# Optimization experiments

Hardware: AMD Instinct MI355X
Metric: run time of the kernel (lower is better)

Reference implementation:

```python
import jax, jax.numpy as jnp
import numpy as np

D = 128   # opt.geometric_latent_dim
H = 132   # FCBlock hidden width (hardcoded in source)
B = 65536
K = 8

def setup_inputs() -> dict:
    key = jax.random.key(0)
    ks = jax.random.split(key, 16)
    s = lambda k, shp, fan: jax.random.normal(k, shp, jnp.float32) / np.sqrt(fan)
    return {
        "signal": jax.random.normal(ks[0], (B, D), jnp.float32),
        "components": jax.random.normal(ks[1], (K, B, D), jnp.float32),
        # message_map / update_map: Linear(D, D)
        "Wm": s(ks[2], (D, D), D), "bm": jnp.zeros((D,), jnp.float32),
        "Wu": s(ks[3], (D, D), D), "bu": jnp.zeros((D,), jnp.float32),
        "W0": s(ks[4], (H, 2 * D), 2 * D), "b0": jnp.zeros((H,), jnp.float32),
        "W1": s(ks[5], (H, H), H),         "b1": jnp.zeros((H,), jnp.float32),
        "W2": s(ks[6], (H, H), H),         "b2": jnp.zeros((H,), jnp.float32),
        "W3": s(ks[7], (D, H), H),         "b3": jnp.zeros((D,), jnp.float32),
    }

def reference(signal, components, Wm, bm, Wu, bu, W0, b0, W1, b1, W2, b2, W3, b3):
    # message_map applied to each component, then summed over components
    msgs = jnp.einsum('kbd,ed->kbe', components, Wm) + bm  # [K,B,D]
    right = msgs.sum(axis=0)                               # [B,D]
    # update_map
    right = right @ Wu.T + bu                              # [B,D]
    # joint_update: FCBlock on concat([signal, right])
    x = jnp.concatenate([signal, right], axis=-1)          # [B,2D]
    x = jax.nn.relu(x @ W0.T + b0)
    x = jax.nn.relu(x @ W1.T + b1)
    x = jax.nn.relu(x @ W2.T + b2)
    return x @ W3.T + b3                                   # [B,D]
```

## Files before the change

### kernel.cpp

```cpp
#include <hip/hip_runtime.h>
#include <stdint.h>

#define DD  128
#define HH  132
#define BB  65536
#define KKC 8
#define HP  144
#define KP  160
#define SW  136
#define SH  168
#define W0S_BYTES 40960
#define WAB_BYTES 81920
#define WH_BYTES  49152
#define ACT_BYTES 43008

typedef short bf16x8 __attribute__((ext_vector_type(8)));
typedef short bf16x4 __attribute__((ext_vector_type(4)));
typedef float f32x4  __attribute__((ext_vector_type(4)));

__device__ __forceinline__ unsigned short f2b(float f){
  union{float f; unsigned u;} c; c.f = f;
  unsigned r = c.u + 0x7fffu + ((c.u >> 16) & 1u);
  return (unsigned short)(r >> 16);
}

__global__ void prepA(const float* __restrict__ Wm, const float* __restrict__ bm,
                      const float* __restrict__ Wu, const float* __restrict__ bu,
                      float* __restrict__ Wf, float* __restrict__ bfv){
  int idx = blockIdx.x * 256 + threadIdx.x;
  int i = idx >> 7, j = idx & 127;
  float acc = 0.f;
  for(int d = 0; d < DD; ++d)
    acc += Wu[i*DD + d] * Wm[d*DD + j];
  Wf[idx] = acc;
  if(j == 0){
    float a = 0.f;
    for(int d = 0; d < DD; ++d) a += Wu[i*DD + d] * bm[d];
    bfv[i] = (float)KKC * a + bu[i];
  }
}

__global__ void prepB(const float* __restrict__ W0, const float* __restrict__ b0,
                      const float* __restrict__ W1, const float* __restrict__ b1,
                      const float* __restrict__ W2, const float* __restrict__ b2,
                      const float* __restrict__ W3, const float* __restrict__ b3,
                      const float* __restrict__ Wf, const float* __restrict__ bfv,
                      unsigned short* __restrict__ wAB,
                      unsigned short* __restrict__ w1p, unsigned short* __restrict__ w2p,
                      unsigned short* __restrict__ w3p,
                      float* __restrict__ b0p, float* __restrict__ b1p,
                      float* __restrict__ b2p, float* __restrict__ b3p){
  int idx = blockIdx.x * 256 + threadIdx.x;
  if(idx < 20480){
    int n = idx / SW, c = idx % SW;
    wAB[idx] = (n < HH && c < DD) ? f2b(W0[n*(2*DD) + c]) : (unsigned short)0;
    return;
  }
  idx -= 20480;
  if(idx < 20480){
    int n = idx / SW, c = idx % SW;
    float acc = 0.f;
    bool live = (n < HH && c < DD);
    if(live)
      for(int i = 0; i < DD; ++i)
        acc += W0[n*(2*DD) + DD + i] * Wf[i*DD + c];
    wAB[20480 + idx] = live ? f2b(acc) : (unsigned short)0;
    return;
  }
  idx -= 20480;
  if(idx < 24576){
    int n = idx / SH, c = idx % SH;
    w1p[idx] = (n < HH && c < HH) ? f2b(W1[n*HH + c]) : (unsigned short)0;
    return;
  }
  idx -= 24576;
  if(idx < 24576){
    int n = idx / SH, c = idx % SH;
    w2p[idx] = (n < HH && c < HH) ? f2b(W2[n*HH + c]) : (unsigned short)0;
    return;
  }
  idx -= 24576;
  if(idx < 24576){
    int n = idx / SH, c = idx % SH;
    w3p[idx] = (n < DD && c < HH) ? f2b(W3[n*HH + c]) : (unsigned short)0;
    return;
  }
  idx -= 24576;
  if(idx < HP){
    float acc = 0.f;
    if(idx < HH){
      acc = b0[idx];
      for(int i = 0; i < DD; ++i) acc += W0[idx*(2*DD) + DD + i] * bfv[i];
    }
    b0p[idx] = acc;
    return;
  }
  idx -= HP;
  if(idx < HP){ b1p[idx] = (idx < HH) ? b1[idx] : 0.f; return; }
  idx -= HP;
  if(idx < HP){ b2p[idx] = (idx < HH) ? b2[idx] : 0.f; return; }
  idx -= HP;
  if(idx < DD){ b3p[idx] = b3[idx]; return; }
}

__global__ __launch_bounds__(256) void comp_sum(
    const float* __restrict__ comps, unsigned short* __restrict__ sumb){
  const size_t base = (size_t)blockIdx.x * 8192;
  const int t = threadIdx.x;
  f32x4 acc[8];
  #pragma unroll
  for(int i = 0; i < 8; ++i) acc[i] = (f32x4){0.f,0.f,0.f,0.f};
  #pragma unroll
  for(int k = 0; k < KKC; ++k){
    const float* p = comps + (size_t)k * BB * DD + base + t*4;
    #pragma unroll
    for(int i = 0; i < 8; ++i) acc[i] += *(const f32x4*)(p + i*1024);
  }
  unsigned short* q = sumb + base + t*4;
  #pragma unroll
  for(int i = 0; i < 8; ++i){
    bf16x4 pk;
    #pragma unroll
    for(int j = 0; j < 4; ++j) pk[j] = (short)f2b(acc[i][j]);
    *(bf16x4*)(q + i*1024) = pk;
  }
}

__global__ __launch_bounds__(512, 2) void fused_mlp(
    const float* __restrict__ signal,
    const unsigned short* __restrict__ sumb,
    const unsigned short* __restrict__ wAB,
    const unsigned short* __restrict__ w1p,
    const unsigned short* __restrict__ w2p,
    const unsigned short* __restrict__ w3p,
    const float* __restrict__ b0p, const float* __restrict__ b1p,
    const float* __restrict__ b2p, const float* __restrict__ b3p,
    float* __restrict__ out)
{
  __shared__ __align__(16) unsigned char ldsbuf[WAB_BYTES + ACT_BYTES];
  unsigned short* ldsAB = (unsigned short*)ldsbuf;
  unsigned short* ldsW  = (unsigned short*)ldsbuf;
  unsigned short* actB  = (unsigned short*)(ldsbuf + WAB_BYTES);

  const int t    = threadIdx.x;
  const int lane = t & 63;
  const int wave = t >> 6;
  const int m    = lane & 15;
  const int quad = lane >> 4;
  const int rowBase = blockIdx.x * 128 + wave * 16;
  const int arow = rowBase + m;
  unsigned short* actW = actB + wave * 16 * SH;

  for(int z = t; z < 8*16*16; z += 512){
    int wv = z >> 8, r = (z >> 4) & 15, c = z & 15;
    actB[(wv*16 + r)*SH + 144 + c] = 0;
  }

  bf16x8 sumf[4];
  #pragma unroll
  for(int ki = 0; ki < 4; ++ki)
    sumf[ki] = *(const bf16x8*)(sumb + (size_t)arow*DD + ki*32 + quad*8);

  f32x4 sl[8];
  {
    const float* srow = signal + (size_t)arow * DD;
    #pragma unroll
    for(int ki = 0; ki < 4; ++ki){
      sl[2*ki]   = *(const f32x4*)(srow + ki*32 + quad*8);
      sl[2*ki+1] = *(const f32x4*)(srow + ki*32 + quad*8 + 4);
    }
  }

  f32x4 rAB[10];
  {
    const f32x4* g = (const f32x4*)wAB;
    #pragma unroll
    for(int c = 0; c < 10; ++c) rAB[c] = g[c*512 + t];
  }

  bf16x8 sigf[4];
  #pragma unroll
  for(int ki = 0; ki < 4; ++ki){
    bf16x8 p;
    #pragma unroll
    for(int j = 0; j < 4; ++j){ p[j] = (short)f2b(sl[2*ki][j]); p[4+j] = (short)f2b(sl[2*ki+1][j]); }
    sigf[ki] = p;
  }

  {
    f32x4* l = (f32x4*)ldsAB;
    #pragma unroll
    for(int c = 0; c < 10; ++c) l[c*512 + t] = rAB[c];
  }
  __syncthreads();

  f32x4 rW[6];
  {
    const f32x4* g = (const f32x4*)w1p;
    #pragma unroll
    for(int c = 0; c < 6; ++c) rW[c] = g[c*512 + t];
  }

  #pragma unroll
  for(int nt = 0; nt < 9; ++nt){
    f32x4 acc = {0.f,0.f,0.f,0.f};
    const int rb = nt*16 + m;
    #pragma unroll
    for(int ki = 0; ki < 4; ++ki){
      bf16x8 wf = *(const bf16x8*)(ldsAB + rb*SW + ki*32 + quad*8);
      acc = __builtin_amdgcn_mfma_f32_16x16x32_bf16(sigf[ki], wf, acc, 0, 0, 0);
    }
    #pragma unroll
    for(int ki = 0; ki < 4; ++ki){
      bf16x8 wf = *(const bf16x8*)(ldsAB + 20480 + rb*SW + ki*32 + quad*8);
      acc = __builtin_amdgcn_mfma_f32_16x16x32_bf16(sumf[ki], wf, acc, 0, 0, 0);
    }
    float bias = b0p[rb];
    #pragma unroll
    for(int r = 0; r < 4; ++r){
      float v = acc[r] + bias;
      v = v > 0.f ? v : 0.f;
      actW[(quad*4 + r)*SH + rb] = f2b(v);
    }
  }
  __syncthreads();

  { f32x4* l = (f32x4*)ldsW;
    #pragma unroll
    for(int c = 0; c < 6; ++c) l[c*512 + t] = rW[c]; }
  __syncthreads();

  bf16x8 hf[5];

  { const f32x4* g = (const f32x4*)w2p;
    #pragma unroll
    for(int c = 0; c < 6; ++c) rW[c] = g[c*512 + t]; }
  #pragma unroll
  for(int ki = 0; ki < 5; ++ki)
    hf[ki] = *(const bf16x8*)(actW + m*SH + ki*32 + quad*8);
  #pragma unroll
  for(int nt = 0; nt < 9; ++nt){
    f32x4 acc = {0.f,0.f,0.f,0.f};
    const int rb = nt*16 + m;
    #pragma unroll
    for(int ki = 0; ki < 5; ++ki){
      bf16x8 wf = *(const bf16x8*)(ldsW + rb*SH + ki*32 + quad*8);
      acc = __builtin_amdgcn_mfma_f32_16x16x32_bf16(hf[ki], wf, acc, 0, 0, 0);
    }
    float bias = b1p[rb];
    #pragma unroll
    for(int r = 0; r < 4; ++r){
      float v = acc[r] + bias;
      v = v > 0.f ? v : 0.f;
      actW[(quad*4 + r)*SH + rb] = f2b(v);
    }
  }
  __syncthreads();

  { f32x4* l = (f32x4*)ldsW;
    #pragma unroll
    for(int c = 0; c < 6; ++c) l[c*512 + t] = rW[c]; }
  __syncthreads();

  { const f32x4* g = (const f32x4*)w3p;
    #pragma unroll
    for(int c = 0; c < 6; ++c) rW[c] = g[c*512 + t]; }
  #pragma unroll
  for(int ki = 0; ki < 5; ++ki)
    hf[ki] = *(const bf16x8*)(actW + m*SH + ki*32 + quad*8);
  #pragma unroll
  for(int nt = 0; nt < 9; ++nt){
    f32x4 acc = {0.f,0.f,0.f,0.f};
    const int rb = nt*16 + m;
    #pragma unroll
    for(int ki = 0; ki < 5; ++ki){
      bf16x8 wf = *(const bf16x8*)(ldsW + rb*SH + ki*32 + quad*8);
      acc = __builtin_amdgcn_mfma_f32_16x16x32_bf16(hf[ki], wf, acc, 0, 0, 0);
    }
    float bias = b2p[rb];
    #pragma unroll
    for(int r = 0; r < 4; ++r){
      float v = acc[r] + bias;
      v = v > 0.f ? v : 0.f;
      actW[(quad*4 + r)*SH + rb] = f2b(v);
    }
  }
  __syncthreads();

  { f32x4* l = (f32x4*)ldsW;
    #pragma unroll
    for(int c = 0; c < 6; ++c) l[c*512 + t] = rW[c]; }
  __syncthreads();

  #pragma unroll
  for(int ki = 0; ki < 5; ++ki)
    hf[ki] = *(const bf16x8*)(actW + m*SH + ki*32 + quad*8);
  #pragma unroll
  for(int nt = 0; nt < 8; ++nt){
    f32x4 acc = {0.f,0.f,0.f,0.f};
    const int rb = nt*16 + m;
    #pragma unroll
    for(int ki = 0; ki < 5; ++ki){
      bf16x8 wf = *(const bf16x8*)(ldsW + rb*SH + ki*32 + quad*8);
      acc = __builtin_amdgcn_mfma_f32_16x16x32_bf16(hf[ki], wf, acc, 0, 0, 0);
    }
    float bias = b3p[rb];
    #pragma unroll
    for(int r = 0; r < 4; ++r){
      int grow = rowBase + quad*4 + r;
      out[(size_t)grow*DD + rb] = acc[r] + bias;
    }
  }
}

extern "C" void kernel_launch(void* const* d_in, const int* in_sizes, int n_in,
                              void* d_out, int out_size, void* d_ws, size_t ws_size,
                              hipStream_t stream){
  const float* signal = (const float*)d_in[0];
  const float* comps  = (const float*)d_in[1];
  const float* Wm = (const float*)d_in[2];
  const float* bm = (const float*)d_in[3];
  const float* Wu = (const float*)d_in[4];
  const float* bu = (const float*)d_in[5];
  const float* W0 = (const float*)d_in[6];
  const float* b0 = (const float*)d_in[7];
  const float* W1 = (const float*)d_in[8];
  const float* b1 = (const float*)d_in[9];
  const float* W2 = (const float*)d_in[10];
  const float* b2 = (const float*)d_in[11];
  const float* W3 = (const float*)d_in[12];
  const float* b3 = (const float*)d_in[13];

  char* ws = (char*)d_ws;
  float*          Wf   = (float*)(ws + 0);
  float*          bfv  = (float*)(ws + 65536);
  unsigned short* wAB  = (unsigned short*)(ws + 66048);
  unsigned short* w1p  = (unsigned short*)(ws + 147968);
  unsigned short* w2p  = (unsigned short*)(ws + 197120);
  unsigned short* w3p  = (unsigned short*)(ws + 246272);
  float*          b0p  = (float*)(ws + 295424);
  float*          b1p  = (float*)(ws + 296000);
  float*          b2p  = (float*)(ws + 296576);
  float*          b3p  = (float*)(ws + 297152);
  unsigned short* sumb = (unsigned short*)(ws + 297728);

  hipLaunchKernelGGL(prepA, dim3(64), dim3(256), 0, stream, Wm, bm, Wu, bu, Wf, bfv);

  hipLaunchKernelGGL(prepB, dim3(451), dim3(256), 0, stream,
                     W0, b0, W1, b1, W2, b2, W3, b3, Wf, bfv,
                     wAB, w1p, w2p, w3p, b0p, b1p, b2p, b3p);

  hipLaunchKernelGGL(comp_sum, dim3(BB*DD/8192), dim3(256), 0, stream, comps, sumb);

  hipLaunchKernelGGL(fused_mlp, dim3(BB/128), dim3(512), 0, stream,
                     signal, sumb, wAB, w1p, w2p, w3p,
                     b0p, b1p, b2p, b3p, (float*)d_out);
}
```

Before: 450.7 us.

## Fuse component sum into MLP kernel and stream weights via async LDS loads

Removes the separate comp_sum kernel and its bf16 intermediate buffer. The fused MLP kernel now reads and sums the K component rows directly. Weights are staged into LDS in 48-row chunks using global_load_lds with double buffering, so loads overlap the MFMA work. This shrinks LDS use to about 70KB, and launch bounds are raised to 4 blocks per CU. Trade-offs are many more __syncthreads per block and heavy per-thread component loads in the main kernel, which may add register pressure or latency.

```diff
diff --git a/kernel.cpp b/kernel.cpp
--- a/kernel.cpp
+++ b/kernel.cpp
@@ -5,14 +5,9 @@
 #define HH  132
 #define BB  65536
 #define KKC 8
-#define HP  144
-#define KP  160
 #define SW  136
 #define SH  168
-#define W0S_BYTES 40960
-#define WAB_BYTES 81920
-#define WH_BYTES  49152
-#define ACT_BYTES 43008
+#define SA  152
 
 typedef short bf16x8 __attribute__((ext_vector_type(8)));
 typedef short bf16x4 __attribute__((ext_vector_type(4)));
@@ -86,7 +81,7 @@
     return;
   }
   idx -= 24576;
-  if(idx < HP){
+  if(idx < 144){
     float acc = 0.f;
     if(idx < HH){
       acc = b0[idx];
@@ -95,40 +90,29 @@
     b0p[idx] = acc;
     return;
   }
-  idx -= HP;
-  if(idx < HP){ b1p[idx] = (idx < HH) ? b1[idx] : 0.f; return; }
-  idx -= HP;
-  if(idx < HP){ b2p[idx] = (idx < HH) ? b2[idx] : 0.f; return; }
-  idx -= HP;
+  idx -= 144;
+  if(idx < 144){ b1p[idx] = (idx < HH) ? b1[idx] : 0.f; return; }
+  idx -= 144;
+  if(idx < 144){ b2p[idx] = (idx < HH) ? b2[idx] : 0.f; return; }
+  idx -= 144;
   if(idx < DD){ b3p[idx] = b3[idx]; return; }
 }
 
-__global__ __launch_bounds__(256) void comp_sum(
-    const float* __restrict__ comps, unsigned short* __restrict__ sumb){
-  const size_t base = (size_t)blockIdx.x * 8192;
-  const int t = threadIdx.x;
-  f32x4 acc[8];
-  #pragma unroll
-  for(int i = 0; i < 8; ++i) acc[i] = (f32x4){0.f,0.f,0.f,0.f};
-  #pragma unroll
-  for(int k = 0; k < KKC; ++k){
-    const float* p = comps + (size_t)k * BB * DD + base + t*4;
-    #pragma unroll
-    for(int i = 0; i < 8; ++i) acc[i] += *(const f32x4*)(p + i*1024);
-  }
-  unsigned short* q = sumb + base + t*4;
-  #pragma unroll
-  for(int i = 0; i < 8; ++i){
-    bf16x4 pk;
-    #pragma unroll
-    for(int j = 0; j < 4; ++j) pk[j] = (short)f2b(acc[i][j]);
-    *(bf16x4*)(q + i*1024) = pk;
-  }
-}
-
-__global__ __launch_bounds__(512, 2) void fused_mlp(
+__device__ __forceinline__ void stage_copy(const void* gsrc, void* ldst,
+                                           int ncalls, int wave, int lane){
+  const unsigned char* g = (const unsigned char*)gsrc + lane*16;
+  unsigned char* l = (unsigned char*)ldst;
+  for(int c = wave; c < ncalls; c += 8){
+    __builtin_amdgcn_global_load_lds(
+      (const __attribute__((address_space(1))) unsigned int*)(g + c*1024),
+      (__attribute__((address_space(3))) unsigned int*)(l + c*1024),
+      16, 0, 0);
+  }
+}
+
+__global__ __launch_bounds__(512, 4) void fused_all(
     const float* __restrict__ signal,
-    const unsigned short* __restrict__ sumb,
+    const float* __restrict__ comps,
     const unsigned short* __restrict__ wAB,
     const unsigned short* __restrict__ w1p,
     const unsigned short* __restrict__ w2p,
@@ -137,10 +121,10 @@
     const float* __restrict__ b2p, const float* __restrict__ b3p,
     float* __restrict__ out)
 {
-  __shared__ __align__(16) unsigned char ldsbuf[WAB_BYTES + ACT_BYTES];
-  unsigned short* ldsAB = (unsigned short*)ldsbuf;
-  unsigned short* ldsW  = (unsigned short*)ldsbuf;
-  unsigned short* actB  = (unsigned short*)(ldsbuf + WAB_BYTES);
+  __shared__ __align__(16) unsigned char lds[71712];
+  unsigned short* R   = (unsigned short*)lds;
+  unsigned short* ACT = (unsigned short*)(lds + 32768);
+  unsigned short* ZB  = (unsigned short*)(lds + 71680);
 
   const int t    = threadIdx.x;
   const int lane = t & 63;
@@ -149,167 +133,142 @@
   const int quad = lane >> 4;
   const int rowBase = blockIdx.x * 128 + wave * 16;
   const int arow = rowBase + m;
-  unsigned short* actW = actB + wave * 16 * SH;
-
-  for(int z = t; z < 8*16*16; z += 512){
-    int wv = z >> 8, r = (z >> 4) & 15, c = z & 15;
-    actB[(wv*16 + r)*SH + 144 + c] = 0;
-  }
-
+  unsigned short* actW = ACT + wave * 16 * SA;
+
+  stage_copy((const char*)wAB,          lds,          13, wave, lane);
+  stage_copy((const char*)wAB + 40960,  lds + 13312,  13, wave, lane);
+
+  f32x4 cs[8];
+  #pragma unroll
+  for(int i = 0; i < 8; ++i) cs[i] = (f32x4){0.f,0.f,0.f,0.f};
+  {
+    const float* crow = comps + (size_t)arow * DD + quad*8;
+    #pragma unroll
+    for(int k = 0; k < KKC; ++k){
+      const float* p = crow + (size_t)k * BB * DD;
+      #pragma unroll
+      for(int ki = 0; ki < 4; ++ki){
+        cs[2*ki]   += *(const f32x4*)(p + ki*32);
+        cs[2*ki+1] += *(const f32x4*)(p + ki*32 + 4);
+      }
+    }
+  }
   bf16x8 sumf[4];
   #pragma unroll
-  for(int ki = 0; ki < 4; ++ki)
-    sumf[ki] = *(const bf16x8*)(sumb + (size_t)arow*DD + ki*32 + quad*8);
-
-  f32x4 sl[8];
+  for(int ki = 0; ki < 4; ++ki){
+    bf16x8 pk;
+    #pragma unroll
+    for(int j = 0; j < 4; ++j){ pk[j] = (short)f2b(cs[2*ki][j]); pk[4+j] = (short)f2b(cs[2*ki+1][j]); }
+    sumf[ki] = pk;
+  }
+
+  bf16x8 sigf[4];
   {
-    const float* srow = signal + (size_t)arow * DD;
+    const float* srow = signal + (size_t)arow * DD + quad*8;
     #pragma unroll
     for(int ki = 0; ki < 4; ++ki){
-      sl[2*ki]   = *(const f32x4*)(srow + ki*32 + quad*8);
-      sl[2*ki+1] = *(const f32x4*)(srow + ki*32 + quad*8 + 4);
-    }
-  }
-
-  f32x4 rAB[10];
+      f32x4 a = *(const f32x4*)(srow + ki*32);
+      f32x4 b = *(const f32x4*)(srow + ki*32 + 4);
+      bf16x8 pk;
+      #pragma unroll
+      for(int j = 0; j < 4; ++j){ pk[j] = (short)f2b(a[j]); pk[4+j] = (short)f2b(b[j]); }
+      sigf[ki] = pk;
+    }
+  }
+
   {
-    const f32x4* g = (const f32x4*)wAB;
-    #pragma unroll
-    for(int c = 0; c < 10; ++c) rAB[c] = g[c*512 + t];
-  }
-
-  bf16x8 sigf[4];
+    int row = t >> 2, p = t & 3;
+    *(unsigned*)(lds + 32768 + row*(SA*2) + 288 + p*4) = 0u;
+    if(t < 8) ((unsigned*)ZB)[t] = 0u;
+  }
+
+  __syncthreads();
+
   #pragma unroll
-  for(int ki = 0; ki < 4; ++ki){
-    bf16x8 p;
-    #pragma unroll
-    for(int j = 0; j < 4; ++j){ p[j] = (short)f2b(sl[2*ki][j]); p[4+j] = (short)f2b(sl[2*ki+1][j]); }
-    sigf[ki] = p;
-  }
-
-  {
-    f32x4* l = (f32x4*)ldsAB;
-    #pragma unroll
-    for(int c = 0; c < 10; ++c) l[c*512 + t] = rAB[c];
-  }
-  __syncthreads();
-
-  f32x4 rW[6];
-  {
-    const f32x4* g = (const f32x4*)w1p;
-    #pragma unroll
-    for(int c = 0; c < 6; ++c) rW[c] = g[c*512 + t];
-  }
-
+  for(int s = 0; s < 3; ++s){
+    #pragma unroll
+    for(int jj = 0; jj < 3; ++jj){
+      const int r  = jj*16 + m;
+      const int rb = s*48 + jj*16 + m;
+      f32x4 acc = {0.f,0.f,0.f,0.f};
+      #pragma unroll
+      for(int ki = 0; ki < 4; ++ki){
+        bf16x8 wf = *(const bf16x8*)(R + r*SW + ki*32 + quad*8);
+        acc = __builtin_amdgcn_mfma_f32_16x16x32_bf16(sigf[ki], wf, acc, 0, 0, 0);
+      }
+      #pragma unroll
+      for(int ki = 0; ki < 4; ++ki){
+        bf16x8 wf = *(const bf16x8*)(R + 6656 + r*SW + ki*32 + quad*8);
+        acc = __builtin_amdgcn_mfma_f32_16x16x32_bf16(sumf[ki], wf, acc, 0, 0, 0);
+      }
+      float bias = b0p[rb];
+      #pragma unroll
+      for(int rr = 0; rr < 4; ++rr){
+        float v = acc[rr] + bias;
+        v = v > 0.f ? v : 0.f;
+        actW[(quad*4 + rr)*SA + rb] = f2b(v);
+      }
+    }
+    __syncthreads();
+    if(s == 0){
+      stage_copy((const char*)wAB + 13056,          lds,         13, wave, lane);
+      stage_copy((const char*)wAB + 40960 + 13056,  lds + 13312, 13, wave, lane);
+    } else if(s == 1){
+      stage_copy((const char*)wAB + 26112,          lds,         13, wave, lane);
+      stage_copy((const char*)wAB + 40960 + 26112,  lds + 13312, 13, wave, lane);
+    } else {
+      stage_copy((const char*)w1p, lds, 16, wave, lane);
+    }
+    __syncthreads();
+  }
+
+  bf16x8 hf[5];
   #pragma unroll
-  for(int nt = 0; nt < 9; ++nt){
-    f32x4 acc = {0.f,0.f,0.f,0.f};
-    const int rb = nt*16 + m;
-    #pragma unroll
-    for(int ki = 0; ki < 4; ++ki){
-      bf16x8 wf = *(const bf16x8*)(ldsAB + rb*SW + ki*32 + quad*8);
-      acc = __builtin_amdgcn_mfma_f32_16x16x32_bf16(sigf[ki], wf, acc, 0, 0, 0);
-    }
-    #pragma unroll
-    for(int ki = 0; ki < 4; ++ki){
-      bf16x8 wf = *(const bf16x8*)(ldsAB + 20480 + rb*SW + ki*32 + quad*8);
-      acc = __builtin_amdgcn_mfma_f32_16x16x32_bf16(sumf[ki], wf, acc, 0, 0, 0);
-    }
-    float bias = b0p[rb];
-    #pragma unroll
-    for(int r = 0; r < 4; ++r){
-      float v = acc[r] + bias;
-      v = v > 0.f ? v : 0.f;
-      actW[(quad*4 + r)*SH + rb] = f2b(v);
-    }
-  }
-  __syncthreads();
-
-  { f32x4* l = (f32x4*)ldsW;
-    #pragma unroll
-    for(int c = 0; c < 6; ++c) l[c*512 + t] = rW[c]; }
-  __syncthreads();
-
-  bf16x8 hf[5];
-
-  { const f32x4* g = (const f32x4*)w2p;
-    #pragma unroll
-    for(int c = 0; c < 6; ++c) rW[c] = g[c*512 + t]; }
-  #pragma unroll
-  for(int ki = 0; ki < 5; ++ki)
-    hf[ki] = *(const bf16x8*)(actW + m*SH + ki*32 + quad*8);
-  #pragma unroll
-  for(int nt = 0; nt < 9; ++nt){
-    f32x4 acc = {0.f,0.f,0.f,0.f};
-    const int rb = nt*16 + m;
-    #pragma unroll
-    for(int ki = 0; ki < 5; ++ki){
-      bf16x8 wf = *(const bf16x8*)(ldsW + rb*SH + ki*32 + quad*8);
-      acc = __builtin_amdgcn_mfma_f32_16x16x32_bf16(hf[ki], wf, acc, 0, 0, 0);
-    }
-    float bias = b1p[rb];
-    #pragma unroll
-    for(int r = 0; r < 4; ++r){
-      float v = acc[r] + bias;
-      v = v > 0.f ? v : 0.f;
-      actW[(quad*4 + r)*SH + rb] = f2b(v);
-    }
-  }
-  __syncthreads();
-
-  { f32x4* l = (f32x4*)ldsW;
-    #pragma unroll
-    for(int c = 0; c < 6; ++c) l[c*512 + t] = rW[c]; }
-  __syncthreads();
-
-  { const f32x4* g = (const f32x4*)w3p;
-    #pragma unroll
-    for(int c = 0; c < 6; ++c) rW[c] = g[c*512 + t]; }
-  #pragma unroll
-  for(int ki = 0; ki < 5; ++ki)
-    hf[ki] = *(const bf16x8*)(actW + m*SH + ki*32 + quad*8);
-  #pragma unroll
-  for(int nt = 0; nt < 9; ++nt){
-    f32x4 acc = {0.f,0.f,0.f,0.f};
-    const int rb = nt*16 + m;
-    #pragma unroll
-    for(int ki = 0; ki < 5; ++ki){
-      bf16x8 wf = *(const bf16x8*)(ldsW + rb*SH + ki*32 + quad*8);
-      acc = __builtin_amdgcn_mfma_f32_16x16x32_bf16(hf[ki], wf, acc, 0, 0, 0);
-    }
-    float bias = b2p[rb];
-    #pragma unroll
-    for(int r = 0; r < 4; ++r){
-      float v = acc[r] + bias;
-      v = v > 0.f ? v : 0.f;
-      actW[(quad*4 + r)*SH + rb] = f2b(v);
-    }
-  }
-  __syncthreads();
-
-  { f32x4* l = (f32x4*)ldsW;
-    #pragma unroll
-    for(int c = 0; c < 6; ++c) l[c*512 + t] = rW[c]; }
-  __syncthreads();
-
-  #pragma unroll
-  for(int ki = 0; ki < 5; ++ki)
-    hf[ki] = *(const bf16x8*)(actW + m*SH + ki*32 + quad*8);
-  #pragma unroll
-  for(int nt = 0; nt < 8; ++nt){
-    f32x4 acc = {0.f,0.f,0.f,0.f};
-    const int rb = nt*16 + m;
-    #pragma unroll
-    for(int ki = 0; ki < 5; ++ki){
-      bf16x8 wf = *(const bf16x8*)(ldsW + rb*SH + ki*32 + quad*8);
-      acc = __builtin_amdgcn_mfma_f32_16x16x32_bf16(hf[ki], wf, acc, 0, 0, 0);
-    }
-    float bias = b3p[rb];
-    #pragma unroll
-    for(int r = 0; r < 4; ++r){
-      int grow = rowBase + quad*4 + r;
-      out[(size_t)grow*DD + rb] = acc[r] + bias;
-    }
+  for(int j = 0; j < 9; ++j){
+    const int layer = j / 3, sub = j - layer*3;
+    if(j < 8){
+      const int nl = (j+1) / 3, ns = (j+1) - nl*3;
+      const unsigned short* src = (nl == 0) ? w1p : (nl == 1) ? w2p : w3p;
+      const int ncalls = (nl == 2 && ns == 2) ? 11 : 16;
+      stage_copy((const char*)src + ns*16128, lds + ((j+1)&1)*16384, ncalls, wave, lane);
+    }
+    if(sub == 0){
+      #pragma unroll
+      for(int ki = 0; ki < 4; ++ki)
+        hf[ki] = *(const bf16x8*)(actW + m*SA + ki*32 + quad*8);
+      const unsigned short* p4 = (quad < 3) ? (actW + m*SA + 128 + quad*8)
+                                            : (const unsigned short*)ZB;
+      hf[4] = *(const bf16x8*)p4;
+    }
+    const unsigned short* W = (const unsigned short*)(lds + (j&1)*16384);
+    const int ntc = (layer == 2 && sub == 2) ? 2 : 3;
+    const float* bias = (layer == 0) ? b1p : (layer == 1) ? b2p : b3p;
+    #pragma unroll
+    for(int jj = 0; jj < 3; ++jj){
+      if(jj < ntc){
+        const int rb = sub*48 + jj*16 + m;
+        f32x4 acc = {0.f,0.f,0.f,0.f};
+        #pragma unroll
+        for(int ki = 0; ki < 5; ++ki){
+          bf16x8 wf = *(const bf16x8*)(W + (jj*16 + m)*SH + ki*32 + quad*8);
+          acc = __builtin_amdgcn_mfma_f32_16x16x32_bf16(hf[ki], wf, acc, 0, 0, 0);
+        }
+        float b = bias[rb];
+        if(layer < 2){
+          #pragma unroll
+          for(int rr = 0; rr < 4; ++rr){
+            float v = acc[rr] + b;
+            v = v > 0.f ? v : 0.f;
+            actW[(quad*4 + rr)*SA + rb] = f2b(v);
+          }
+        } else {
+          #pragma unroll
+          for(int rr = 0; rr < 4; ++rr)
+            out[(size_t)(rowBase + quad*4 + rr)*DD + rb] = acc[rr] + b;
+        }
+      }
+    }
+    __syncthreads();
   }
 }
 
@@ -342,7 +301,6 @@
   float*          b1p  = (float*)(ws + 296000);
   float*          b2p  = (float*)(ws + 296576);
   float*          b3p  = (float*)(ws + 297152);
-  unsigned short* sumb = (unsigned short*)(ws + 297728);
 
   hipLaunchKernelGGL(prepA, dim3(64), dim3(256), 0, stream, Wm, bm, Wu, bu, Wf, bfv);
 
@@ -350,9 +308,7 @@
                      W0, b0, W1, b1, W2, b2, W3, b3, Wf, bfv,
                      wAB, w1p, w2p, w3p, b0p, b1p, b2p, b3p);
 
-  hipLaunchKernelGGL(comp_sum, dim3(BB*DD/8192), dim3(256), 0, stream, comps, sumb);
-
-  hipLaunchKernelGGL(fused_mlp, dim3(BB/128), dim3(512), 0, stream,
-                     signal, sumb, wAB, w1p, w2p, w3p,
+  hipLaunchKernelGGL(fused_all, dim3(BB/128), dim3(512), 0, stream,
+                     signal, comps, wAB, w1p, w2p, w3p,
                      b0p, b1p, b2p, b3p, (float*)d_out);
 }
```

After: 525.9 us. 16.7% more time.
